# Performance work log

Hardware: AMD Instinct MI355X
Metric: run time of the kernel (lower is better)

Reference implementation:

```python
import jax, jax.numpy as jnp
import numpy as np


def setup_inputs() -> dict:
    key = jax.random.key(0)
    kx, kq = jax.random.split(key)
    B, L, D = 4, 4096, 256
    x = jax.random.normal(kx, (B, L, D), dtype=jnp.float32)
    q = jax.random.normal(kq, (D,), dtype=jnp.float32)
    return {"x": x, "q": q}


def reference(x, q):
    # x: [B, L, D], q: [D]
    B, L, D = x.shape
    # scores[b, i, j] = x[b, i] . q  (broadcast query => rank-1 "matmul")
    s = jnp.einsum("bld,d->bl", x, q)                      # [B, L]
    scores = jnp.broadcast_to(s[:, :, None], (B, L, L))    # [B, L, L]
    # causal mask: positions j > i are masked (triu, diagonal=1)
    causal_mask = jnp.triu(jnp.ones((L, L), dtype=bool), k=1)  # [L, L]
    scores = jnp.where(causal_mask[None, :, :], -jnp.inf, scores)
    attn = jax.nn.softmax(scores, axis=-1)                 # [B, L, L]
    pooled = jnp.einsum("blj,bjd->bld", attn, x)           # [B, L, D]
    return pooled
```

## Files before the change

kernel.cpp:

```cpp
#include <hip/hip_runtime.h>


#define LL    4096
#define DD4   64
#define NB    512
#define CHUNK 8
#define COLS4 256
#define GSZ   16
#define NGRP  32

__device__ __forceinline__ void f4add(float4& a, const float4 b) {
    a.x += b.x; a.y += b.y; a.z += b.z; a.w += b.w;
}

__global__ __launch_bounds__(256) void cap_sums(const float* __restrict__ x,
                                                float4* __restrict__ P) {
    const int t = threadIdx.x, c = blockIdx.x;
    const int b = t >> 6, d4 = t & 63;
    const float4* xb = reinterpret_cast<const float4*>(x) + (size_t)b * LL * DD4 + d4;
    const int l0 = c * CHUNK;
    float4 s = {0.f, 0.f, 0.f, 0.f};
#pragma unroll
    for (int k = 0; k < CHUNK; ++k) f4add(s, xb[(size_t)(l0 + k) * DD4]);
    P[c * COLS4 + t] = s;
}

__global__ __launch_bounds__(256) void cap_groups(const float4* __restrict__ P,
                                                  float4* __restrict__ S) {
    const int t = threadIdx.x, g = blockIdx.x;
    float4 s0 = {0.f,0.f,0.f,0.f}, s1 = {0.f,0.f,0.f,0.f};
#pragma unroll
    for (int j = 0; j < GSZ; j += 2) {
        f4add(s0, P[(g * GSZ + j)     * COLS4 + t]);
        f4add(s1, P[(g * GSZ + j + 1) * COLS4 + t]);
    }
    f4add(s0, s1);
    S[g * COLS4 + t] = s0;
}

__global__ __launch_bounds__(256) void cap_out(const float* __restrict__ x,
                                               const float4* __restrict__ P,
                                               const float4* __restrict__ S,
                                               float* __restrict__ out) {
    const int t = threadIdx.x, c = blockIdx.x;
    const int b = t >> 6, d4 = t & 63;
    const size_t colbase = (size_t)b * LL * DD4 + d4;
    const float4* xb = reinterpret_cast<const float4*>(x) + colbase;
    const int l0 = c * CHUNK;

    float4 v[CHUNK];
#pragma unroll
    for (int k = 0; k < CHUNK; ++k) v[k] = xb[(size_t)(l0 + k) * DD4];

    float4 r0 = {0.f,0.f,0.f,0.f}, r1 = {0.f,0.f,0.f,0.f};
    const int G = c >> 4;
#pragma unroll 4
    for (int g = 0; g + 1 < G; g += 2) {
        f4add(r0, S[g * COLS4 + t]);
        f4add(r1, S[(g + 1) * COLS4 + t]);
    }
    if (G & 1) f4add(r0, S[(G - 1) * COLS4 + t]);
#pragma unroll 4
    for (int j = G * GSZ; j < c; ++j) f4add(r1, P[j * COLS4 + t]);
    float4 run = r0; f4add(run, r1);

    float4* ob = reinterpret_cast<float4*>(out) + colbase;
#pragma unroll
    for (int k = 0; k < CHUNK; ++k) {
        f4add(run, v[k]);
        const float inv = 1.0f / (float)(l0 + k + 1);
        float4 o = {run.x * inv, run.y * inv, run.z * inv, run.w * inv};
        ob[(size_t)(l0 + k) * DD4] = o;
    }
}

extern "C" void kernel_launch(void* const* d_in, const int* in_sizes, int n_in,
                              void* d_out, int out_size, void* d_ws, size_t ws_size,
                              hipStream_t stream) {
    const float* x = (const float*)d_in[0];
    float* out = (float*)d_out;
    float4* P  = (float4*)d_ws;
    float4* S  = P + (size_t)NB * COLS4;

    cap_sums  <<<dim3(NB),   dim3(256), 0, stream>>>(x, P);
    cap_groups<<<dim3(NGRP), dim3(256), 0, stream>>>(P, S);
    cap_out   <<<dim3(NB),   dim3(256), 0, stream>>>(x, P, S, out);
}
```

Baseline: 21.30 us.

## Fuse chunk and group prefix sums into one kernel with shared-memory reduction

Merges the per-chunk sum kernel and the group-sum kernel into a single 1024-thread kernel that computes 8-row chunk sums and reduces four of them in shared memory into 32-row super-chunk sums. This removes one kernel launch and the separate pass that re-read chunk sums. In exchange, the output kernel must now add up to 127 super-chunk sums instead of up to 31 group sums, which increases its serial load chain.

```diff
diff --git a/kernel.cpp b/kernel.cpp
--- a/kernel.cpp
+++ b/kernel.cpp
@@ -3,70 +3,68 @@
 
 #define LL    4096
 #define DD4   64
-#define NB    512
-#define CHUNK 8
 #define COLS4 256
-#define GSZ   16
-#define NGRP  32
+#define NSUP  128
+#define SUPR  32
+#define NCH   512
+#define CHR   8
 
 __device__ __forceinline__ void f4add(float4& a, const float4 b) {
     a.x += b.x; a.y += b.y; a.z += b.z; a.w += b.w;
 }
 
-__global__ __launch_bounds__(256) void cap_sums(const float* __restrict__ x,
-                                                float4* __restrict__ P) {
-    const int t = threadIdx.x, c = blockIdx.x;
+__global__ __launch_bounds__(1024) void cap_sums(const float* __restrict__ x,
+                                                 float4* __restrict__ P8,
+                                                 float4* __restrict__ P32) {
+    __shared__ float4 sm[4][COLS4];
+    const int tid = threadIdx.x;
+    const int p = tid >> 8, t = tid & 255;
     const int b = t >> 6, d4 = t & 63;
+    const int c = blockIdx.x;
+    const int l0 = c * SUPR + p * CHR;
     const float4* xb = reinterpret_cast<const float4*>(x) + (size_t)b * LL * DD4 + d4;
-    const int l0 = c * CHUNK;
     float4 s = {0.f, 0.f, 0.f, 0.f};
 #pragma unroll
-    for (int k = 0; k < CHUNK; ++k) f4add(s, xb[(size_t)(l0 + k) * DD4]);
-    P[c * COLS4 + t] = s;
-}
-
-__global__ __launch_bounds__(256) void cap_groups(const float4* __restrict__ P,
-                                                  float4* __restrict__ S) {
-    const int t = threadIdx.x, g = blockIdx.x;
-    float4 s0 = {0.f,0.f,0.f,0.f}, s1 = {0.f,0.f,0.f,0.f};
-#pragma unroll
-    for (int j = 0; j < GSZ; j += 2) {
-        f4add(s0, P[(g * GSZ + j)     * COLS4 + t]);
-        f4add(s1, P[(g * GSZ + j + 1) * COLS4 + t]);
+    for (int k = 0; k < CHR; ++k) f4add(s, xb[(size_t)(l0 + k) * DD4]);
+    P8[(c * 4 + p) * COLS4 + t] = s;
+    sm[p][t] = s;
+    __syncthreads();
+    if (p == 0) {
+        float4 g = sm[0][t];
+        f4add(g, sm[1][t]); f4add(g, sm[2][t]); f4add(g, sm[3][t]);
+        P32[c * COLS4 + t] = g;
     }
-    f4add(s0, s1);
-    S[g * COLS4 + t] = s0;
 }
 
 __global__ __launch_bounds__(256) void cap_out(const float* __restrict__ x,
-                                               const float4* __restrict__ P,
-                                               const float4* __restrict__ S,
+                                               const float4* __restrict__ P8,
+                                               const float4* __restrict__ P32,
                                                float* __restrict__ out) {
     const int t = threadIdx.x, c = blockIdx.x;
     const int b = t >> 6, d4 = t & 63;
     const size_t colbase = (size_t)b * LL * DD4 + d4;
     const float4* xb = reinterpret_cast<const float4*>(x) + colbase;
-    const int l0 = c * CHUNK;
+    const int l0 = c * CHR;
 
-    float4 v[CHUNK];
+    float4 v[CHR];
 #pragma unroll
-    for (int k = 0; k < CHUNK; ++k) v[k] = xb[(size_t)(l0 + k) * DD4];
+    for (int k = 0; k < CHR; ++k) v[k] = xb[(size_t)(l0 + k) * DD4];
 
+    const int SUP = c >> 2;
     float4 r0 = {0.f,0.f,0.f,0.f}, r1 = {0.f,0.f,0.f,0.f};
-    const int G = c >> 4;
 #pragma unroll 4
-    for (int g = 0; g + 1 < G; g += 2) {
-        f4add(r0, S[g * COLS4 + t]);
-        f4add(r1, S[(g + 1) * COLS4 + t]);
+    for (int j = 0; j + 1 < SUP; j += 2) {
+        f4add(r0, P32[j * COLS4 + t]);
+        f4add(r1, P32[(j + 1) * COLS4 + t]);
     }
-    if (G & 1) f4add(r0, S[(G - 1) * COLS4 + t]);
-#pragma unroll 4
-    for (int j = G * GSZ; j < c; ++j) f4add(r1, P[j * COLS4 + t]);
+    if (SUP & 1) f4add(r0, P32[(SUP - 1) * COLS4 + t]);
+#pragma unroll
+    for (int j = SUP * 4; j < c; ++j) f4add(r1, P8[j * COLS4 + t]);
     float4 run = r0; f4add(run, r1);
 
     float4* ob = reinterpret_cast<float4*>(out) + colbase;
 #pragma unroll
-    for (int k = 0; k < CHUNK; ++k) {
+    for (int k = 0; k < CHR; ++k) {
         f4add(run, v[k]);
         const float inv = 1.0f / (float)(l0 + k + 1);
         float4 o = {run.x * inv, run.y * inv, run.z * inv, run.w * inv};
@@ -79,10 +77,9 @@
                               hipStream_t stream) {
     const float* x = (const float*)d_in[0];
     float* out = (float*)d_out;
-    float4* P  = (float4*)d_ws;
-    float4* S  = P + (size_t)NB * COLS4;
+    float4* P8  = (float4*)d_ws;
+    float4* P32 = P8 + (size_t)NCH * COLS4;
 
-    cap_sums  <<<dim3(NB),   dim3(256), 0, stream>>>(x, P);
-    cap_groups<<<dim3(NGRP), dim3(256), 0, stream>>>(P, S);
-    cap_out   <<<dim3(NB),   dim3(256), 0, stream>>>(x, P, S, out);
+    cap_sums<<<dim3(NSUP), dim3(1024), 0, stream>>>(x, P8, P32);
+    cap_out <<<dim3(NCH),  dim3(256),  0, stream>>>(x, P8, P32, out);
 }
```

Result: slower. 22.06 us (+3.6%).
